# Kernel optimization log

Hardware: AMD Instinct MI355X
Metric: run time of the kernel (lower is better)

## Reference

```python
import jax, jax.numpy as jnp
import numpy as np

B = 131072
D = 64
NUM_REL = 32


def setup_inputs() -> dict:
    key = jax.random.key(0)
    k1, k2, k3, k4 = jax.random.split(key, 4)
    embeds1 = jax.random.normal(k1, (B, D), dtype=jnp.float32)
    embeds2 = jax.random.normal(k2, (B, D), dtype=jnp.float32)
    rels = jax.random.randint(k3, (B,), 0, NUM_REL, dtype=jnp.int32)
    # learned relation table: one D*D matrix per relation type
    rel_embeds = jax.random.normal(k4, (NUM_REL, D * D), dtype=jnp.float32)
    return {"embeds1": embeds1, "embeds2": embeds2, "rels": rels,
            "rel_embeds": rel_embeds}


def reference(embeds1, embeds2, rels, rel_embeds):
    # gather per-sample relation matrices: [B, D, D]
    rel_mats = rel_embeds[rels].reshape(-1, D, D)
    # per-sample bilinear form: score_b = e1_b^T R_b e2_b  -> [B]
    e1R = jnp.einsum("bd,bde->be", embeds1, rel_mats)
    return (e1R * embeds2).sum(axis=1)
```

## Files before the change

kernel.cpp:

```cpp
#include <hip/hip_runtime.h>
#include <hip/hip_bf16.h>
#include <cstddef>

#define BB 131072
#define DD 64
#define NREL 32
#define PADN 133120
#define NWAVE (PADN / 64)

#define BLOCKS_AC 512
#define SPB (BB / BLOCKS_AC)
#define CHUNKS 8
#define BPC (BLOCKS_AC / CHUNKS)

typedef __attribute__((ext_vector_type(8))) __bf16 bf16x8;
typedef __attribute__((ext_vector_type(16))) float f32x16;

__global__ __launch_bounds__(256) void phaseA_hist(
    const int* __restrict__ rels, int* __restrict__ blockCnt,
    int* __restrict__ permPacked) {
  __shared__ int hist[NREL];
  const int t = threadIdx.x;
  if (t < NREL) hist[t] = 0;
  __syncthreads();
  const int gid = blockIdx.x * 256 + t;
  permPacked[gid] = -1;
  if (gid < PADN - BB) permPacked[BB + gid] = -1;
  atomicAdd(&hist[rels[gid]], 1);
  __syncthreads();
  if (t < NREL) blockCnt[blockIdx.x * NREL + t] = hist[t];
}

__global__ __launch_bounds__(256) void phaseB_scan(
    const int* __restrict__ blockCnt, int* __restrict__ blockOff,
    int* __restrict__ binBase) {
  __shared__ int partial[CHUNKS][NREL];
  __shared__ int chunkBase[CHUNKS][NREL];
  __shared__ int binB[NREL];
  const int t = threadIdx.x;
  const int c = t >> 5;
  const int r = t & 31;
  const int b0 = c * BPC;
  int run = 0;
#pragma unroll 4
  for (int b = 0; b < BPC; ++b) run += blockCnt[(b0 + b) * NREL + r];
  partial[c][r] = run;
  __syncthreads();
  if (t < NREL) {
    int acc = 0;
#pragma unroll
    for (int i = 0; i < CHUNKS; ++i) { chunkBase[i][t] = acc; acc += partial[i][t]; }
  }
  __syncthreads();
  if (t == 0) {
    int acc = 0;
#pragma unroll
    for (int i = 0; i < NREL; ++i) {
      binB[i] = acc;
      const int tot = chunkBase[CHUNKS - 1][i] + partial[CHUNKS - 1][i];
      acc += (tot + 63) & ~63;
    }
  }
  __syncthreads();
  if (t < NREL) binBase[t] = binB[t];
  int run2 = chunkBase[c][r];
#pragma unroll 4
  for (int b = 0; b < BPC; ++b) {
    blockOff[(b0 + b) * NREL + r] = run2;
    run2 += blockCnt[(b0 + b) * NREL + r];
  }
}

__global__ __launch_bounds__(256) void phaseC_scatter(
    const int* __restrict__ rels, const int* __restrict__ blockOff,
    const int* __restrict__ binBase, int* __restrict__ permPacked) {
  __shared__ int cnt[NREL];
  __shared__ int baseArr[NREL];
  const int t = threadIdx.x;
  if (t < NREL) {
    cnt[t] = 0;
    baseArr[t] = binBase[t] + blockOff[blockIdx.x * NREL + t];
  }
  __syncthreads();
  const int s = blockIdx.x * SPB + t;
  const int rv = rels[s];
  const int rank = atomicAdd(&cnt[rv], 1);
  permPacked[baseArr[rv] + rank] = (rv << 17) | s;
}

__global__ __launch_bounds__(64) void bilinear_mfma(
    const float* __restrict__ e1g, const float* __restrict__ e2g,
    const float* __restrict__ relE, const int* __restrict__ permPacked,
    float* __restrict__ out) {
  __shared__ float sA[DD * 65];
  const int lane = threadIdx.x;
  const int pk = permPacked[blockIdx.x * 64 + lane];
  const unsigned long long vm = __ballot(pk >= 0);
  if (vm == 0ull) return;
  const int fv = (int)__builtin_ctzll(vm);
  const int r0 = __builtin_amdgcn_readlane(pk, fv) >> 17;
  const int h = lane >> 5;
  const int l31 = lane & 31;

#pragma unroll
  for (int i = 0; i < DD; ++i) {
    const int bi = __builtin_amdgcn_readlane(pk, i) & 0x1FFFF;
    sA[i * 65 + lane] = e1g[(size_t)bi * DD + lane];
  }
  __syncthreads();

  const float* __restrict__ R = relE + (size_t)r0 * (DD * DD);

  f32x16 acc[2][2];
#pragma unroll
  for (int ti = 0; ti < 2; ++ti)
#pragma unroll
    for (int tj = 0; tj < 2; ++tj)
#pragma unroll
      for (int i = 0; i < 16; ++i) acc[ti][tj][i] = 0.f;

#pragma unroll
  for (int kc = 0; kc < 4; ++kc) {
    bf16x8 aH[2], aL[2], bH[2], bL[2];
#pragma unroll
    for (int ti = 0; ti < 2; ++ti) {
      const float* p = &sA[(32 * ti + l31) * 65 + kc * 16 + 8 * h];
#pragma unroll
      for (int j = 0; j < 8; ++j) {
        const float x = p[j];
        const __bf16 hb = (__bf16)x;
        const float lo = x - (float)hb;
        aH[ti][j] = hb;
        aL[ti][j] = (__bf16)lo;
      }
    }
#pragma unroll
    for (int tj = 0; tj < 2; ++tj) {
      const float* q = R + (size_t)(kc * 16 + 8 * h) * DD + 32 * tj + l31;
#pragma unroll
      for (int j = 0; j < 8; ++j) {
        const float x = q[(size_t)j * DD];
        const __bf16 hb = (__bf16)x;
        const float lo = x - (float)hb;
        bH[tj][j] = hb;
        bL[tj][j] = (__bf16)lo;
      }
    }
#pragma unroll
    for (int ti = 0; ti < 2; ++ti)
#pragma unroll
      for (int tj = 0; tj < 2; ++tj) {
        acc[ti][tj] = __builtin_amdgcn_mfma_f32_32x32x16_bf16(aH[ti], bH[tj], acc[ti][tj], 0, 0, 0);
        acc[ti][tj] = __builtin_amdgcn_mfma_f32_32x32x16_bf16(aH[ti], bL[tj], acc[ti][tj], 0, 0, 0);
        acc[ti][tj] = __builtin_amdgcn_mfma_f32_32x32x16_bf16(aL[ti], bH[tj], acc[ti][tj], 0, 0, 0);
      }
  }

  float rp[32];
#pragma unroll
  for (int i = 0; i < 32; ++i) rp[i] = 0.f;
#pragma unroll
  for (int ti = 0; ti < 2; ++ti)
#pragma unroll
    for (int g = 0; g < 4; ++g)
#pragma unroll
      for (int q = 0; q < 4; ++q) {
        const int reg = g * 4 + q;
        const int rbase = 32 * ti + q + 8 * g;
        const int s0 = __builtin_amdgcn_readlane(pk, rbase) & 0x1FFFF;
        const int s1 = __builtin_amdgcn_readlane(pk, rbase + 4) & 0x1FFFF;
        const int bs = h ? s1 : s0;
        const float* er = e2g + (size_t)bs * DD + l31;
        rp[ti * 16 + reg] = fmaf(acc[ti][0][reg], er[0],
                            fmaf(acc[ti][1][reg], er[32], rp[ti * 16 + reg]));
      }

  __syncthreads();
  float* sP = sA;
#pragma unroll
  for (int ti = 0; ti < 2; ++ti)
#pragma unroll
    for (int g = 0; g < 4; ++g)
#pragma unroll
      for (int q = 0; q < 4; ++q) {
        const int row = 32 * ti + q + 8 * g + 4 * h;
        sP[row * 33 + l31] = rp[ti * 16 + g * 4 + q];
      }
  __syncthreads();
  float sc = 0.f;
#pragma unroll
  for (int c = 0; c < 32; ++c) sc += sP[lane * 33 + c];
  if (pk >= 0) out[pk & 0x1FFFF] = sc;
}

extern "C" void kernel_launch(void* const* d_in, const int* in_sizes, int n_in,
                              void* d_out, int out_size, void* d_ws, size_t ws_size,
                              hipStream_t stream) {
  const float* e1 = (const float*)d_in[0];
  const float* e2 = (const float*)d_in[1];
  const int* rels = (const int*)d_in[2];
  const float* relE = (const float*)d_in[3];
  float* out = (float*)d_out;

  int* permPacked = (int*)d_ws;
  int* blockCnt = permPacked + PADN;
  int* blockOff = blockCnt + BLOCKS_AC * NREL;
  int* binBase = blockOff + BLOCKS_AC * NREL;

  phaseA_hist<<<BLOCKS_AC, 256, 0, stream>>>(rels, blockCnt, permPacked);
  phaseB_scan<<<1, 256, 0, stream>>>(blockCnt, blockOff, binBase);
  phaseC_scatter<<<BLOCKS_AC, 256, 0, stream>>>(rels, blockOff, binBase, permPacked);
  bilinear_mfma<<<NWAVE, 64, 0, stream>>>(e1, e2, relE, permPacked, out);
}
```

Before: 112.5 us.

## Pre-split relation matrices into bf16 hi/lo MFMA layout and load A directly

Adds a pre-pass kernel that converts each relation matrix once into bf16 high and low parts, stored in the exact per-lane B-operand layout the MFMA wants, so the main kernel loads them as vector reads instead of doing strided scalar fp32 loads and splitting them per wave. The e1 rows are now read straight from global memory as float4 pairs, with no shared-memory staging or barrier, and split on the fly. The cost is one extra kernel launch and workspace traffic for the preprocessed table. The A loads become per-lane row gathers, so coalescing depends on how the cache handles them.

```diff
diff --git a/kernel.cpp b/kernel.cpp
--- a/kernel.cpp
+++ b/kernel.cpp
@@ -15,6 +15,28 @@
 
 typedef __attribute__((ext_vector_type(8))) __bf16 bf16x8;
 typedef __attribute__((ext_vector_type(16))) float f32x16;
+
+__global__ __launch_bounds__(256) void phaseR_pre(
+    const float* __restrict__ relE, __bf16* __restrict__ Rpre) {
+  const int r = blockIdx.x >> 3;
+  const int seg = blockIdx.x & 7;
+  const int t = threadIdx.x;
+  const float* __restrict__ R = relE + (size_t)r * (DD * DD);
+  __bf16* __restrict__ dst = Rpre + (size_t)r * 8192;
+#pragma unroll
+  for (int i = 0; i < 2; ++i) {
+    const int idx = seg * 512 + i * 256 + t;
+    const int grp = idx >> 9;
+    const int lane = (idx >> 3) & 63;
+    const int j = idx & 7;
+    const int k = (grp >> 1) * 16 + (lane >> 5) * 8 + j;
+    const int n = (grp & 1) * 32 + (lane & 31);
+    const float x = R[k * DD + n];
+    const __bf16 hb = (__bf16)x;
+    dst[idx] = hb;
+    dst[4096 + idx] = (__bf16)(x - (float)hb);
+  }
+}
 
 __global__ __launch_bounds__(256) void phaseA_hist(
     const int* __restrict__ rels, int* __restrict__ blockCnt,
@@ -88,11 +110,22 @@
   permPacked[baseArr[rv] + rank] = (rv << 17) | s;
 }
 
+__device__ __forceinline__ void split8(const float4 v0, const float4 v1,
+                                       bf16x8& hi, bf16x8& lo) {
+  const float x[8] = {v0.x, v0.y, v0.z, v0.w, v1.x, v1.y, v1.z, v1.w};
+#pragma unroll
+  for (int j = 0; j < 8; ++j) {
+    const __bf16 hb = (__bf16)x[j];
+    hi[j] = hb;
+    lo[j] = (__bf16)(x[j] - (float)hb);
+  }
+}
+
 __global__ __launch_bounds__(64) void bilinear_mfma(
     const float* __restrict__ e1g, const float* __restrict__ e2g,
-    const float* __restrict__ relE, const int* __restrict__ permPacked,
+    const __bf16* __restrict__ Rpre, const int* __restrict__ permPacked,
     float* __restrict__ out) {
-  __shared__ float sA[DD * 65];
+  __shared__ float sP[DD * 33];
   const int lane = threadIdx.x;
   const int pk = permPacked[blockIdx.x * 64 + lane];
   const unsigned long long vm = __ballot(pk >= 0);
@@ -102,14 +135,10 @@
   const int h = lane >> 5;
   const int l31 = lane & 31;
 
-#pragma unroll
-  for (int i = 0; i < DD; ++i) {
-    const int bi = __builtin_amdgcn_readlane(pk, i) & 0x1FFFF;
-    sA[i * 65 + lane] = e1g[(size_t)bi * DD + lane];
-  }
-  __syncthreads();
-
-  const float* __restrict__ R = relE + (size_t)r0 * (DD * DD);
+  const int s0 = __shfl(pk, l31) & 0x1FFFF;
+  const int s1 = __shfl(pk, 32 + l31) & 0x1FFFF;
+
+  const bf16x8* __restrict__ bp = (const bf16x8*)(Rpre + (size_t)r0 * 8192);
 
   f32x16 acc[2][2];
 #pragma unroll
@@ -123,28 +152,16 @@
   for (int kc = 0; kc < 4; ++kc) {
     bf16x8 aH[2], aL[2], bH[2], bL[2];
 #pragma unroll
+    for (int tj = 0; tj < 2; ++tj) {
+      const int grp = kc * 2 + tj;
+      bH[tj] = bp[grp * 64 + lane];
+      bL[tj] = bp[512 + grp * 64 + lane];
+    }
+#pragma unroll
     for (int ti = 0; ti < 2; ++ti) {
-      const float* p = &sA[(32 * ti + l31) * 65 + kc * 16 + 8 * h];
-#pragma unroll
-      for (int j = 0; j < 8; ++j) {
-        const float x = p[j];
-        const __bf16 hb = (__bf16)x;
-        const float lo = x - (float)hb;
-        aH[ti][j] = hb;
-        aL[ti][j] = (__bf16)lo;
-      }
-    }
-#pragma unroll
-    for (int tj = 0; tj < 2; ++tj) {
-      const float* q = R + (size_t)(kc * 16 + 8 * h) * DD + 32 * tj + l31;
-#pragma unroll
-      for (int j = 0; j < 8; ++j) {
-        const float x = q[(size_t)j * DD];
-        const __bf16 hb = (__bf16)x;
-        const float lo = x - (float)hb;
-        bH[tj][j] = hb;
-        bL[tj][j] = (__bf16)lo;
-      }
+      const int s = ti ? s1 : s0;
+      const float4* ap = (const float4*)(e1g + (size_t)s * DD + kc * 16 + 8 * h);
+      split8(ap[0], ap[1], aH[ti], aL[ti]);
     }
 #pragma unroll
     for (int ti = 0; ti < 2; ++ti)
@@ -167,16 +184,15 @@
       for (int q = 0; q < 4; ++q) {
         const int reg = g * 4 + q;
         const int rbase = 32 * ti + q + 8 * g;
-        const int s0 = __builtin_amdgcn_readlane(pk, rbase) & 0x1FFFF;
-        const int s1 = __builtin_amdgcn_readlane(pk, rbase + 4) & 0x1FFFF;
-        const int bs = h ? s1 : s0;
+        const int sa = __builtin_amdgcn_readlane(pk, rbase) & 0x1FFFF;
+        const int sb = __builtin_amdgcn_readlane(pk, rbase + 4) & 0x1FFFF;
+        const int bs = h ? sb : sa;
         const float* er = e2g + (size_t)bs * DD + l31;
         rp[ti * 16 + reg] = fmaf(acc[ti][0][reg], er[0],
                             fmaf(acc[ti][1][reg], er[32], rp[ti * 16 + reg]));
       }
 
   __syncthreads();
-  float* sP = sA;
 #pragma unroll
   for (int ti = 0; ti < 2; ++ti)
 #pragma unroll
@@ -206,9 +222,11 @@
   int* blockCnt = permPacked + PADN;
   int* blockOff = blockCnt + BLOCKS_AC * NREL;
   int* binBase = blockOff + BLOCKS_AC * NREL;
-
+  __bf16* Rpre = (__bf16*)((char*)d_ws + (1 << 20));
+
+  phaseR_pre<<<NREL * 8, 256, 0, stream>>>(relE, Rpre);
   phaseA_hist<<<BLOCKS_AC, 256, 0, stream>>>(rels, blockCnt, permPacked);
   phaseB_scan<<<1, 256, 0, stream>>>(blockCnt, blockOff, binBase);
   phaseC_scatter<<<BLOCKS_AC, 256, 0, stream>>>(rels, blockOff, binBase, permPacked);
-  bilinear_mfma<<<NWAVE, 64, 0, stream>>>(e1, e2, relE, permPacked, out);
-}
+  bilinear_mfma<<<NWAVE, 64, 0, stream>>>(e1, e2, Rpre, permPacked, out);
+}
```

New measurement: 120.7 us. 7.3% more time.
